# Kernel optimization log

Hardware: AMD Instinct MI355X
Metric: run time of the kernel (lower is better)

The kernel has to match this reference:

```python
import jax, jax.numpy as jnp
import numpy as np

# ---- model dims (match init_kwargs) ----
N_PER = 10000          # nodes per omic view
NUM_OMICS = 3
N = N_PER * NUM_OMICS  # 30000 total nodes (omic blocks are contiguous)
E = 500000             # edges
R = 6                  # num_relations
HEADS = 1
PROJ = 128             # proj_dim
H0 = 128               # hidden_channels[0]
H1 = 128               # hidden_channels[1]
LABELS = 5
IN_SIZES = [2000, 1500, 1000]
SLOPE = 0.2            # RGATConv leaky_relu negative_slope


def setup_inputs() -> dict:
    key = jax.random.key(0)
    ks = iter(jax.random.split(key, 64))

    def nrm(shape, fan_in):
        return jax.random.normal(next(ks), shape, dtype=jnp.float32) / np.float32(np.sqrt(fan_in))

    inp = {}
    for i, s in enumerate(IN_SIZES):
        inp[f"x{i}"] = jax.random.normal(next(ks), (N_PER, s), dtype=jnp.float32)
    for i, s in enumerate(IN_SIZES):
        inp[f"projW{i}"] = nrm((s, PROJ), s)
        inp[f"projb{i}"] = jnp.zeros((PROJ,), jnp.float32)
    for i in range(NUM_OMICS):
        inp[f"slW{i}"] = nrm((PROJ, H0), PROJ)
        inp[f"slb{i}"] = jnp.zeros((H0,), jnp.float32)
    # RGAT layer 1: weight [R, in, heads*out], q/k [heads*out, heads], bias [heads*out]
    inp["W1"] = nrm((R, PROJ, HEADS * H0), PROJ)
    inp["q1"] = nrm((HEADS * H0, HEADS), H0)
    inp["k1"] = nrm((HEADS * H0, HEADS), H0)
    inp["b1"] = jnp.zeros((HEADS * H0,), jnp.float32)
    # RGAT layer 2: heads=1
    inp["W2"] = nrm((R, HEADS * H0, H1), H0)
    inp["q2"] = nrm((H1, 1), H1)
    inp["k2"] = nrm((H1, 1), H1)
    inp["b2"] = jnp.zeros((H1,), jnp.float32)
    inp["lin1W"] = nrm((H1, H1), H1)
    inp["lin1b"] = jnp.zeros((H1,), jnp.float32)
    inp["lin2W"] = nrm((H1, LABELS), H1)
    inp["lin2b"] = jnp.zeros((LABELS,), jnp.float32)
    inp["edge_src"] = jax.random.randint(next(ks), (E,), 0, N, dtype=jnp.int32)
    inp["edge_dst"] = jax.random.randint(next(ks), (E,), 0, N, dtype=jnp.int32)
    inp["edge_type"] = jax.random.randint(next(ks), (E,), 0, R, dtype=jnp.int32)
    return inp


def _rgat(x, src, dst, etype, W, q, k, b, heads, out_ch):
    """PyG RGATConv: additive-self-attention, across-relation softmax, mod='f-scaled'."""
    # per-relation linear transform of all nodes, then gather per edge
    xw = jnp.einsum('nd,rdo->rno', x, W)          # [R, N, heads*out]
    out_i = xw[etype, dst]                        # [E, heads*out] (target)
    out_j = xw[etype, src]                        # [E, heads*out] (source)
    alpha = jax.nn.leaky_relu(out_i @ q + out_j @ k, SLOPE)   # [E, heads]
    # segment softmax over destination nodes
    m = jax.ops.segment_max(alpha, dst, num_segments=N)
    a = jnp.exp(alpha - m[dst])
    s = jax.ops.segment_sum(a, dst, num_segments=N)
    a = a / s[dst]
    # f-scaled: multiply by in-degree of destination
    deg = jax.ops.segment_sum(jnp.ones((a.shape[0],), a.dtype), dst, num_segments=N)
    a = a * deg[dst][:, None]
    msg = (a[:, :, None] * out_j.reshape(-1, heads, out_ch)).reshape(-1, heads * out_ch)
    return jax.ops.segment_sum(msg, dst, num_segments=N) + b


def reference(x0, x1, x2, projW0, projb0, projW1, projb1, projW2, projb2,
              slW0, slb0, slW1, slb1, slW2, slb2,
              W1, q1, k1, b1, W2, q2, k2, b2,
              lin1W, lin1b, lin2W, lin2b,
              edge_src, edge_dst, edge_type):
    # per-omic projections (ELU)
    xp0 = jax.nn.elu(x0 @ projW0 + projb0)
    xp1 = jax.nn.elu(x1 @ projW1 + projb1)
    xp2 = jax.nn.elu(x2 @ projW2 + projb2)
    x = jnp.concatenate([xp0, xp1, xp2], axis=0)  # [N, PROJ] homogeneous features
    # self-loop contributions (self_loops1 is applied after BOTH convs, on projected x,
    # as in the original forward). Omic node blocks are contiguous.
    sl = jnp.concatenate([xp0 @ slW0 + slb0, xp1 @ slW1 + slb1, xp2 @ slW2 + slb2], axis=0)
    h = jax.nn.elu(_rgat(x, edge_src, edge_dst, edge_type, W1, q1, k1, b1, HEADS, H0) + sl)
    h = jax.nn.elu(_rgat(h, edge_src, edge_dst, edge_type, W2, q2, k2, b2, 1, H1) + sl)
    # classify node_type == 0 nodes (first omic block); dropout p=0.2 is identity at eval
    z = jax.nn.elu(h[:N_PER] @ lin1W + lin1b)
    return z @ lin2W + lin2b
```

## Files before the change

kernel.cpp:

```cpp
#include <hip/hip_runtime.h>
#include <math.h>

#define N_TOTAL 30000
#define NPER 10000
#define NEDGE 500000
#define NREL 6
#define SLOPE 0.2f
#define MAXDEG 256

typedef __attribute__((ext_vector_type(4))) float f32x4;
typedef __attribute__((ext_vector_type(8))) short s16x8;
typedef __attribute__((ext_vector_type(4))) short s16x4;
typedef unsigned short u16;
typedef unsigned int u32;

__device__ __forceinline__ u16 f2bf(float v) {
  u32 x = __float_as_uint(v);
  u32 r = (x + 0x7fffu + ((x >> 16) & 1u)) >> 16;
  return (u16)r;
}
__device__ __forceinline__ float bf2f(u16 u) {
  return __uint_as_float(((u32)u) << 16);
}

struct GB {
  const float* A[3];
  const u16* Bt[3];
  const float* bias[3];
  const float* add[3];
  float* C[3];
  int K[3];
  int Kp[3];
};

template<bool BIAS, bool ELU, bool ADD>
__global__ __launch_bounds__(256, 2)
void gemm_mfma(GB gb, int M)
{
  __shared__ char As[64 * 128];
  __shared__ char Aslo[64 * 128];
  __shared__ char Bs[128 * 128];
  const int z = blockIdx.z;
  const int K = gb.K[z], Kp = gb.Kp[z];
  const int tid = threadIdx.x;
  const int bm = blockIdx.x * 64;
  const int lane = tid & 63;
  const int wave = tid >> 6;
  const int wr = wave >> 1, wc = wave & 1;
  const int lane16 = lane & 15, lhalf = lane >> 4;
  const float* A = gb.A[z];
  const u16* Bt = gb.Bt[z];

  f32x4 acc[2][4];
  #pragma unroll
  for (int mi = 0; mi < 2; mi++)
    #pragma unroll
    for (int ni = 0; ni < 4; ni++)
      #pragma unroll
      for (int q = 0; q < 4; q++) acc[mi][ni][q] = 0.f;

  for (int k0 = 0; k0 < Kp; k0 += 64) {
    #pragma unroll
    for (int it = 0; it < 4; it++) {
      int idx = tid + it * 256;
      int row = idx >> 4;
      int kc = (idx & 15) << 2;
      int gr = bm + row, gk = k0 + kc;
      float4 v = make_float4(0.f, 0.f, 0.f, 0.f);
      if (gr < M && gk < K) v = *(const float4*)&A[(size_t)gr * K + gk];
      s16x4 hi, lo;
      float vv[4] = {v.x, v.y, v.z, v.w};
      #pragma unroll
      for (int j = 0; j < 4; j++) {
        u16 h = f2bf(vv[j]);
        hi[j] = (short)h;
        lo[j] = (short)f2bf(vv[j] - bf2f(h));
      }
      int boff = row * 128 + ((kc * 2) ^ ((row & 7) << 4));
      *(s16x4*)(As + boff) = hi;
      *(s16x4*)(Aslo + boff) = lo;
    }
    #pragma unroll
    for (int it = 0; it < 4; it++) {
      int idx = tid + it * 256;
      int row = idx >> 3;
      int kc = (idx & 7) << 3;
      s16x8 v = *(const s16x8*)&Bt[(size_t)row * Kp + k0 + kc];
      *(s16x8*)(Bs + row * 128 + ((kc * 2) ^ ((row & 7) << 4))) = v;
    }
    __syncthreads();
    #pragma unroll
    for (int kk = 0; kk < 2; kk++) {
      const int kbyte = kk * 64 + lhalf * 16;
      s16x8 afh[2], afl[2], bfr[4];
      #pragma unroll
      for (int mi = 0; mi < 2; mi++) {
        int row = wr * 32 + mi * 16 + lane16;
        int boff = row * 128 + (kbyte ^ ((row & 7) << 4));
        afh[mi] = *(const s16x8*)(As + boff);
        afl[mi] = *(const s16x8*)(Aslo + boff);
      }
      #pragma unroll
      for (int ni = 0; ni < 4; ni++) {
        int row = wc * 64 + ni * 16 + lane16;
        bfr[ni] = *(const s16x8*)(Bs + row * 128 + (kbyte ^ ((row & 7) << 4)));
      }
      #pragma unroll
      for (int mi = 0; mi < 2; mi++)
        #pragma unroll
        for (int ni = 0; ni < 4; ni++) {
          acc[mi][ni] = __builtin_amdgcn_mfma_f32_16x16x32_bf16(
              afl[mi], bfr[ni], acc[mi][ni], 0, 0, 0);
          acc[mi][ni] = __builtin_amdgcn_mfma_f32_16x16x32_bf16(
              afh[mi], bfr[ni], acc[mi][ni], 0, 0, 0);
        }
    }
    __syncthreads();
  }

  float bcol[4];
  #pragma unroll
  for (int ni = 0; ni < 4; ni++) {
    int col = wc * 64 + ni * 16 + lane16;
    if (BIAS) bcol[ni] = gb.bias[z][col];
  }
  #pragma unroll
  for (int mi = 0; mi < 2; mi++) {
    #pragma unroll
    for (int q = 0; q < 4; q++) {
      int grow = bm + wr * 32 + mi * 16 + lhalf * 4 + q;
      if (grow < M) {
        #pragma unroll
        for (int ni = 0; ni < 4; ni++) {
          float v = acc[mi][ni][q];
          int col = wc * 64 + ni * 16 + lane16;
          if (BIAS) v += bcol[ni];
          if (ADD) v += gb.add[z][(size_t)grow * 128 + col];
          if (ELU) v = v > 0.f ? v : expm1f(v);
          gb.C[z][(size_t)grow * 128 + col] = v;
        }
      }
    }
  }
}

struct SK {
  const float* A[3];
  const u16* Bt[3];
  float* C[3];
  int K[3];
  int Kp[3];
};

__global__ __launch_bounds__(256, 2)
void gemm_splitk(SK sk, int M)
{
  __shared__ char As[64 * 128];
  __shared__ char Aslo[64 * 128];
  __shared__ char Bs[128 * 128];
  const int z = blockIdx.z;
  const int K = sk.K[z], Kp = sk.Kp[z];
  const int cb = blockIdx.y * 512;
  if (cb >= Kp) return;
  const int kend = (cb + 512 < Kp) ? cb + 512 : Kp;
  const int tid = threadIdx.x;
  const int bm = blockIdx.x * 64;
  const int lane = tid & 63;
  const int wave = tid >> 6;
  const int wr = wave >> 1, wc = wave & 1;
  const int lane16 = lane & 15, lhalf = lane >> 4;
  const float* A = sk.A[z];
  const u16* Bt = sk.Bt[z];

  f32x4 acc[2][4];
  #pragma unroll
  for (int mi = 0; mi < 2; mi++)
    #pragma unroll
    for (int ni = 0; ni < 4; ni++)
      #pragma unroll
      for (int q = 0; q < 4; q++) acc[mi][ni][q] = 0.f;

  for (int k0 = cb; k0 < kend; k0 += 64) {
    #pragma unroll
    for (int it = 0; it < 4; it++) {
      int idx = tid + it * 256;
      int row = idx >> 4;
      int kc = (idx & 15) << 2;
      int gr = bm + row, gk = k0 + kc;
      float4 v = make_float4(0.f, 0.f, 0.f, 0.f);
      if (gr < M && gk < K) v = *(const float4*)&A[(size_t)gr * K + gk];
      s16x4 hi, lo;
      float vv[4] = {v.x, v.y, v.z, v.w};
      #pragma unroll
      for (int j = 0; j < 4; j++) {
        u16 h = f2bf(vv[j]);
        hi[j] = (short)h;
        lo[j] = (short)f2bf(vv[j] - bf2f(h));
      }
      int boff = row * 128 + ((kc * 2) ^ ((row & 7) << 4));
      *(s16x4*)(As + boff) = hi;
      *(s16x4*)(Aslo + boff) = lo;
    }
    #pragma unroll
    for (int it = 0; it < 4; it++) {
      int idx = tid + it * 256;
      int row = idx >> 3;
      int kc = (idx & 7) << 3;
      s16x8 v = *(const s16x8*)&Bt[(size_t)row * Kp + k0 + kc];
      *(s16x8*)(Bs + row * 128 + ((kc * 2) ^ ((row & 7) << 4))) = v;
    }
    __syncthreads();
    #pragma unroll
    for (int kk = 0; kk < 2; kk++) {
      const int kbyte = kk * 64 + lhalf * 16;
      s16x8 afh[2], afl[2], bfr[4];
      #pragma unroll
      for (int mi = 0; mi < 2; mi++) {
        int row = wr * 32 + mi * 16 + lane16;
        int boff = row * 128 + (kbyte ^ ((row & 7) << 4));
        afh[mi] = *(const s16x8*)(As + boff);
        afl[mi] = *(const s16x8*)(Aslo + boff);
      }
      #pragma unroll
      for (int ni = 0; ni < 4; ni++) {
        int row = wc * 64 + ni * 16 + lane16;
        bfr[ni] = *(const s16x8*)(Bs + row * 128 + (kbyte ^ ((row & 7) << 4)));
      }
      #pragma unroll
      for (int mi = 0; mi < 2; mi++)
        #pragma unroll
        for (int ni = 0; ni < 4; ni++) {
          acc[mi][ni] = __builtin_amdgcn_mfma_f32_16x16x32_bf16(
              afl[mi], bfr[ni], acc[mi][ni], 0, 0, 0);
          acc[mi][ni] = __builtin_amdgcn_mfma_f32_16x16x32_bf16(
              afh[mi], bfr[ni], acc[mi][ni], 0, 0, 0);
        }
    }
    __syncthreads();
  }

  float* C = sk.C[z] + (size_t)blockIdx.y * M * 128;
  #pragma unroll
  for (int mi = 0; mi < 2; mi++) {
    #pragma unroll
    for (int q = 0; q < 4; q++) {
      int grow = bm + wr * 32 + mi * 16 + lhalf * 4 + q;
      if (grow < M) {
        #pragma unroll
        for (int ni = 0; ni < 4; ni++) {
          int col = wc * 64 + ni * 16 + lane16;
          C[(size_t)grow * 128 + col] = acc[mi][ni][q];
        }
      }
    }
  }
}

struct RP { const float* bias[3]; int nch[3]; };

__global__ __launch_bounds__(256)
void reduce_proj(const float* __restrict__ part, RP rp, float* __restrict__ Xf)
{
  int z = blockIdx.z;
  int i = blockIdx.x * 256 + threadIdx.x;
  int c = i & 127;
  int nch = rp.nch[z];
  const float* base = part + (size_t)z * 4 * NPER * 128 + i;
  float s = 0.f;
  for (int ch = 0; ch < nch; ch++) s += base[(size_t)ch * NPER * 128];
  s += rp.bias[z][c];
  Xf[(size_t)z * NPER * 128 + i] = s > 0.f ? s : expm1f(s);
}

struct CW {
  const float* src[9];
  u16* dst[9];
  int K[9];
  int Kp[9];
};

__global__ __launch_bounds__(256)
void conv_w(CW cw) {
  int z = blockIdx.z;
  int K = cw.K[z], Kp = cw.Kp[z];
  int idx = blockIdx.x * 256 + threadIdx.x;
  if (idx >= 128 * Kp) return;
  int kq = idx >> 7, n = idx & 127;
  cw.dst[z][(size_t)n * Kp + kq] =
      (kq < K) ? f2bf(cw.src[z][(size_t)kq * 128 + n]) : (u16)0;
}

__global__ __launch_bounds__(128)
void wqk_kernel(const float* __restrict__ W, const float* __restrict__ q,
                const float* __restrict__ k, float* __restrict__ wq,
                float* __restrict__ wk)
{
  int r = blockIdx.x;
  int t = threadIdx.x;
  const float* Wr = W + (size_t)r * 128 * 128 + (size_t)t * 128;
  float aq = 0.f, ak = 0.f;
  for (int o = 0; o < 128; o++) {
    float w = Wr[o];
    aq = fmaf(w, q[o], aq);
    ak = fmaf(w, k[o], ak);
  }
  wq[r * 128 + t] = aq;
  wk[r * 128 + t] = ak;
}

__global__ __launch_bounds__(256)
void qdkd_kernel(const float* __restrict__ Xf, const float* __restrict__ wq,
                 const float* __restrict__ wk, float* __restrict__ QD,
                 float* __restrict__ KD)
{
  __shared__ float sq[NREL * 128], sk[NREL * 128];
  for (int i = threadIdx.x; i < NREL * 128; i += 256) { sq[i] = wq[i]; sk[i] = wk[i]; }
  __syncthreads();
  int n = blockIdx.x * 256 + threadIdx.x;
  if (n >= N_TOTAL) return;
  float aq[NREL], ak[NREL];
  #pragma unroll
  for (int r = 0; r < NREL; r++) { aq[r] = 0.f; ak[r] = 0.f; }
  for (int kc = 0; kc < 128; kc += 4) {
    float4 x = *(const float4*)&Xf[(size_t)n * 128 + kc];
    #pragma unroll
    for (int r = 0; r < NREL; r++) {
      aq[r] += x.x * sq[r * 128 + kc] + x.y * sq[r * 128 + kc + 1]
             + x.z * sq[r * 128 + kc + 2] + x.w * sq[r * 128 + kc + 3];
      ak[r] += x.x * sk[r * 128 + kc] + x.y * sk[r * 128 + kc + 1]
             + x.z * sk[r * 128 + kc + 2] + x.w * sk[r * 128 + kc + 3];
    }
  }
  #pragma unroll
  for (int r = 0; r < NREL; r++) {
    QD[(size_t)r * N_TOTAL + n] = aq[r];
    KD[(size_t)r * N_TOTAL + n] = ak[r];
  }
}

__global__ __launch_bounds__(256)
void edge_count(const int* __restrict__ dst, int* __restrict__ cnt) {
  int e = blockIdx.x * 256 + threadIdx.x;
  if (e < NEDGE) atomicAdd(&cnt[dst[e]], 1);
}

__global__ __launch_bounds__(1024)
void scan_kernel(const int* __restrict__ cnt, int* __restrict__ off,
                 int* __restrict__ cur) {
  __shared__ int ps[1024];
  const int t = threadIdx.x;
  const int CH = (N_TOTAL + 1023) / 1024;
  const int base = t * CH;
  int s = 0;
  for (int i = 0; i < CH; i++) {
    int idx = base + i;
    if (idx < N_TOTAL) s += cnt[idx];
  }
  ps[t] = s;
  __syncthreads();
  for (int o = 1; o < 1024; o <<= 1) {
    int v = (t >= o) ? ps[t - o] : 0;
    __syncthreads();
    ps[t] += v;
    __syncthreads();
  }
  int run = ps[t] - s;
  for (int i = 0; i < CH; i++) {
    int idx = base + i;
    if (idx < N_TOTAL) {
      off[idx] = run; cur[idx] = run;
      run += cnt[idx];
    }
  }
  if (t == 1023) off[N_TOTAL] = run;
}

__global__ __launch_bounds__(256)
void edge_fill(const int* __restrict__ dst, int* __restrict__ cur,
               int* __restrict__ csre) {
  int e = blockIdx.x * 256 + threadIdx.x;
  if (e >= NEDGE) return;
  int p = atomicAdd(&cur[dst[e]], 1);
  csre[p] = e;
}

__device__ __forceinline__ float block_max2(float v, float* red, int tid) {
  #pragma unroll
  for (int m = 32; m; m >>= 1) v = fmaxf(v, __shfl_xor(v, m));
  if ((tid & 63) == 0) red[tid >> 6] = v;
  __syncthreads();
  return fmaxf(red[0], red[1]);
}
__device__ __forceinline__ float block_sum2(float v, float* red, int tid) {
  #pragma unroll
  for (int m = 32; m; m >>= 1) v += __shfl_xor(v, m);
  if ((tid & 63) == 0) red[tid >> 6] = v;
  __syncthreads();
  return red[0] + red[1];
}

__global__ __launch_bounds__(128)
void csr_agg2(const int* __restrict__ off, const int* __restrict__ csre,
              const int* __restrict__ src, const int* __restrict__ et,
              const float* __restrict__ qd, const float* __restrict__ kd,
              const float* __restrict__ xrow, float* __restrict__ agg)
{
  __shared__ float al[MAXDEG];
  __shared__ int2 st[MAXDEG];
  __shared__ float redm[2], reds[2];
  __shared__ float qrow[NREL];
  const int d = blockIdx.x;
  const int tid = threadIdx.x;
  const int n0 = off[d];
  const int deg = off[d + 1] - n0;
  float accr[NREL] = {0.f, 0.f, 0.f, 0.f, 0.f, 0.f};

  if (deg > 0) {
    if (tid < NREL) qrow[tid] = qd[tid * N_TOTAL + d];
    __syncthreads();
    const bool fits = (deg <= MAXDEG);
    float lmax = -3.0e38f;
    for (int i = tid; i < deg; i += 128) {
      int e = csre[n0 + i];
      int t = et[e], s_ = src[e];
      float a = qrow[t] + kd[t * N_TOTAL + s_];
      a = (a > 0.f) ? a : SLOPE * a;
      if (fits) { al[i] = a; st[i] = make_int2(t, s_); }
      lmax = fmaxf(lmax, a);
    }
    __syncthreads();
    const float m = block_max2(lmax, redm, tid);
    float lsum = 0.f;
    for (int i = tid; i < deg; i += 128) {
      float a;
      if (fits) a = al[i];
      else {
        int e = csre[n0 + i];
        a = qrow[et[e]] + kd[et[e] * N_TOTAL + src[e]];
        a = (a > 0.f) ? a : SLOPE * a;
      }
      lsum += expf(a - m);
    }
    const float ssum = block_sum2(lsum, reds, tid);
    const float scale = (float)deg / ssum;
    if (fits) {
      for (int i = tid; i < deg; i += 128)
        al[i] = expf(al[i] - m) * scale;
    }
    __syncthreads();
    if (fits) {
      int i = 0;
      for (; i + 1 < deg; i += 2) {
        float c0 = al[i], c1 = al[i + 1];
        int2 e0 = st[i], e1 = st[i + 1];
        float v0 = xrow[(size_t)e0.y * 128 + tid];
        float v1 = xrow[(size_t)e1.y * 128 + tid];
        float cv0 = c0 * v0, cv1 = c1 * v1;
        #pragma unroll
        for (int r = 0; r < NREL; r++) {
          accr[r] += (e0.x == r) ? cv0 : 0.f;
          accr[r] += (e1.x == r) ? cv1 : 0.f;
        }
      }
      if (i < deg) {
        int2 e0 = st[i];
        float cv0 = al[i] * xrow[(size_t)e0.y * 128 + tid];
        #pragma unroll
        for (int r = 0; r < NREL; r++) accr[r] += (e0.x == r) ? cv0 : 0.f;
      }
    } else {
      for (int i = 0; i < deg; i++) {
        int e = csre[n0 + i];
        int t = et[e], s_ = src[e];
        float a = qrow[t] + kd[t * N_TOTAL + s_];
        a = (a > 0.f) ? a : SLOPE * a;
        float cv = expf(a - m) * scale * xrow[(size_t)s_ * 128 + tid];
        #pragma unroll
        for (int r = 0; r < NREL; r++) accr[r] += (t == r) ? cv : 0.f;
      }
    }
  }
  #pragma unroll
  for (int r = 0; r < NREL; r++)
    agg[((size_t)d * NREL + r) * 128 + tid] = accr[r];
}

__global__ __launch_bounds__(256)
void lin2_kernel(const float* __restrict__ z, const float* __restrict__ W,
                 const float* __restrict__ b, float* __restrict__ out)
{
  int row = blockIdx.x * 4 + (threadIdx.x >> 6);
  int lane = threadIdx.x & 63;
  if (row >= NPER) return;
  float p[5] = {0.f, 0.f, 0.f, 0.f, 0.f};
  #pragma unroll
  for (int h = 0; h < 2; h++) {
    int kidx = lane + h * 64;
    float zv = z[(size_t)row * 128 + kidx];
    #pragma unroll
    for (int j = 0; j < 5; j++) p[j] = fmaf(zv, W[kidx * 5 + j], p[j]);
  }
  #pragma unroll
  for (int mm = 32; mm; mm >>= 1)
    #pragma unroll
    for (int j = 0; j < 5; j++) p[j] += __shfl_xor(p[j], mm);
  if (lane == 0) {
    #pragma unroll
    for (int j = 0; j < 5; j++) out[(size_t)row * 5 + j] = p[j] + b[j];
  }
}

extern "C" void kernel_launch(void* const* d_in, const int* in_sizes, int n_in,
                              void* d_out, int out_size, void* d_ws, size_t ws_size,
                              hipStream_t stream) {
  const float* xs[3] = {(const float*)d_in[0], (const float*)d_in[1], (const float*)d_in[2]};
  const float* projW[3] = {(const float*)d_in[3], (const float*)d_in[5], (const float*)d_in[7]};
  const float* projb[3] = {(const float*)d_in[4], (const float*)d_in[6], (const float*)d_in[8]};
  const float* slW[3]   = {(const float*)d_in[9], (const float*)d_in[11], (const float*)d_in[13]};
  const float* slb[3]   = {(const float*)d_in[10], (const float*)d_in[12], (const float*)d_in[14]};
  const float* W1 = (const float*)d_in[15];
  const float* q1 = (const float*)d_in[16];
  const float* k1 = (const float*)d_in[17];
  const float* b1 = (const float*)d_in[18];
  const float* W2 = (const float*)d_in[19];
  const float* q2 = (const float*)d_in[20];
  const float* k2 = (const float*)d_in[21];
  const float* b2 = (const float*)d_in[22];
  const float* lin1W = (const float*)d_in[23];
  const float* lin1b = (const float*)d_in[24];
  const float* lin2W = (const float*)d_in[25];
  const float* lin2b = (const float*)d_in[26];
  const int* esrc = (const int*)d_in[27];
  const int* edst = (const int*)d_in[28];
  const int* etyp = (const int*)d_in[29];

  char* wp = (char*)d_ws;
  auto alloc = [&](size_t bytes) -> char* {
    char* p = wp; wp += (bytes + 255) & ~(size_t)255; return p;
  };
  float* Xf  = (float*)alloc((size_t)N_TOTAL * 128 * 4);
  float* SL  = (float*)alloc((size_t)N_TOTAL * 128 * 4);
  float* Hf  = (float*)alloc((size_t)N_TOTAL * 128 * 4);
  float* QD  = (float*)alloc((size_t)NREL * N_TOTAL * 4);
  float* KD  = (float*)alloc((size_t)NREL * N_TOTAL * 4);
  float* Z   = (float*)alloc((size_t)NPER * 128 * 4);
  float* WQ1 = (float*)alloc((size_t)NREL * 128 * 4);
  float* WK1 = (float*)alloc((size_t)NREL * 128 * 4);
  float* WQ2 = (float*)alloc((size_t)NREL * 128 * 4);
  float* WK2 = (float*)alloc((size_t)NREL * 128 * 4);
  int*   CNT = (int*)  alloc((size_t)N_TOTAL * 4);
  int*   OFF = (int*)  alloc((size_t)(N_TOTAL + 1) * 4);
  int*   CUR = (int*)  alloc((size_t)N_TOTAL * 4);
  int*   CSRE= (int*)  alloc((size_t)NEDGE * 4);

  float* AGG  = (float*)alloc((size_t)N_TOTAL * NREL * 128 * 4);
  float* PART = AGG;

  CW cw;
  int nW = 0;
  auto addW = [&](const float* src, int K) {
    int Kp = (K + 63) & ~63;
    cw.src[nW] = src; cw.K[nW] = K; cw.Kp[nW] = Kp;
    cw.dst[nW] = (u16*)alloc((size_t)128 * Kp * 2);
    nW++;
  };
  addW(projW[0], 2000); addW(projW[1], 1500); addW(projW[2], 1000);
  addW(slW[0], 128); addW(slW[1], 128); addW(slW[2], 128);
  addW(W1, NREL * 128);
  addW(W2, NREL * 128);
  addW(lin1W, 128);

  const int gridM_per = (NPER + 63) / 64;
  const int gridM_tot = (N_TOTAL + 63) / 64;
  const int gridE = (NEDGE + 255) / 256;

  hipMemsetAsync(CNT, 0, (size_t)N_TOTAL * 4, stream);
  edge_count<<<gridE, 256, 0, stream>>>(edst, CNT);
  scan_kernel<<<1, 1024, 0, stream>>>(CNT, OFF, CUR);
  edge_fill<<<gridE, 256, 0, stream>>>(edst, CUR, CSRE);

  conv_w<<<dim3(1024, 1, 9), 256, 0, stream>>>(cw);
  wqk_kernel<<<NREL, 128, 0, stream>>>(W1, q1, k1, WQ1, WK1);
  wqk_kernel<<<NREL, 128, 0, stream>>>(W2, q2, k2, WQ2, WK2);

  {
    SK sk;
    for (int z = 0; z < 3; z++) {
      sk.A[z] = xs[z]; sk.Bt[z] = cw.dst[z];
      sk.C[z] = PART + (size_t)z * 4 * NPER * 128;
      sk.K[z] = cw.K[z]; sk.Kp[z] = cw.Kp[z];
    }
    gemm_splitk<<<dim3(gridM_per, 4, 3), 256, 0, stream>>>(sk, NPER);
    RP rp;
    for (int z = 0; z < 3; z++) { rp.bias[z] = projb[z]; rp.nch[z] = cw.Kp[z] / 512; }
    reduce_proj<<<dim3(NPER * 128 / 256, 1, 3), 256, 0, stream>>>(PART, rp, Xf);
  }
  {
    GB g;
    for (int z = 0; z < 3; z++) {
      g.A[z] = Xf + (size_t)z * NPER * 128; g.Bt[z] = cw.dst[3 + z];
      g.bias[z] = slb[z]; g.add[z] = nullptr;
      g.C[z] = SL + (size_t)z * NPER * 128;
      g.K[z] = 128; g.Kp[z] = 128;
    }
    gemm_mfma<true, false, false><<<dim3(gridM_per, 1, 3), 256, 0, stream>>>(g, NPER);
  }

  for (int layer = 0; layer < 2; layer++) {
    const float* Ain = (layer == 0) ? Xf : Hf;
    const float* WQ = (layer == 0) ? WQ1 : WQ2;
    const float* WK = (layer == 0) ? WK1 : WK2;
    const float* bb = (layer == 0) ? b1 : b2;
    const u16* Wstk = cw.dst[6 + layer];

    qdkd_kernel<<<(N_TOTAL + 255) / 256, 256, 0, stream>>>(Ain, WQ, WK, QD, KD);
    csr_agg2<<<N_TOTAL, 128, 0, stream>>>(OFF, CSRE, esrc, etyp, QD, KD, Ain, AGG);
    GB g;
    g.A[0] = AGG; g.Bt[0] = Wstk; g.bias[0] = bb; g.add[0] = SL; g.C[0] = Hf;
    g.K[0] = NREL * 128; g.Kp[0] = NREL * 128;
    gemm_mfma<true, true, true><<<dim3(gridM_tot, 1, 1), 256, 0, stream>>>(g, N_TOTAL);
  }

  {
    GB g;
    g.A[0] = Hf; g.Bt[0] = cw.dst[8]; g.bias[0] = lin1b; g.add[0] = nullptr; g.C[0] = Z;
    g.K[0] = 128; g.Kp[0] = 128;
    gemm_mfma<true, true, false><<<dim3(gridM_per, 1, 1), 256, 0, stream>>>(g, NPER);
  }
  lin2_kernel<<<(NPER + 3) / 4, 256, 0, stream>>>(Z, lin2W, lin2b, (float*)d_out);
}
```

Before: 501.9 us.

## Prefetch GEMM tiles into registers, pack edge metadata, wave-per-node aggregation

The GEMM body moves into a shared core that loads the next K-tile from global memory into registers while the current tile is computed, overlapping memory latency with MFMA work. The CSR fill now stores the source index and edge type packed into one int, which removes the indirect loads of src and etype during aggregation. Aggregation switches from one 128-thread block per node to one 64-lane wave per node, with wave-level shuffles for the softmax and float2 feature loads, so no shared memory or block barriers are needed. The packing assumes node ids fit in 15 bits; 30000 does, but only just. Adds register pressure, and degrees above 256 take a slower three-pass path.

Result: faster. 432.9 us (-13.7%).

```diff
diff --git a/kernel.cpp b/kernel.cpp
--- a/kernel.cpp
+++ b/kernel.cpp
@@ -6,7 +6,7 @@
 #define NEDGE 500000
 #define NREL 6
 #define SLOPE 0.2f
-#define MAXDEG 256
+#define WCAP 4
 
 typedef __attribute__((ext_vector_type(4))) float f32x4;
 typedef __attribute__((ext_vector_type(8))) short s16x8;
@@ -21,6 +21,133 @@
 }
 __device__ __forceinline__ float bf2f(u16 u) {
   return __uint_as_float(((u32)u) << 16);
+}
+
+template<bool BIAS, bool ELU, bool ADD, bool SPLITK>
+__device__ __forceinline__ void gemm_core(
+    const float* __restrict__ A, const u16* __restrict__ Bt,
+    const float* __restrict__ bias, const float* __restrict__ add,
+    float* __restrict__ C, int M, int K, int Kp, int kbeg, int kend)
+{
+  __shared__ char As[64 * 128];
+  __shared__ char Aslo[64 * 128];
+  __shared__ char Bs[128 * 128];
+  const int tid = threadIdx.x;
+  const int bm = blockIdx.x * 64;
+  const int lane = tid & 63;
+  const int wave = tid >> 6;
+  const int wr = wave >> 1, wc = wave & 1;
+  const int lane16 = lane & 15, lhalf = lane >> 4;
+
+  const int a_row0 = tid >> 4;
+  const int a_kc = (tid & 15) << 2;
+  const int b_row0 = tid >> 3;
+  const int b_kc = (tid & 7) << 3;
+
+  float4 pa[4];
+  s16x8 pb[4];
+
+  auto LOAD = [&](int k0) {
+    #pragma unroll
+    for (int it = 0; it < 4; it++) {
+      int gr = bm + a_row0 + it * 16, gk = k0 + a_kc;
+      float4 v = make_float4(0.f, 0.f, 0.f, 0.f);
+      if (gr < M && gk < K) v = *(const float4*)&A[(size_t)gr * K + gk];
+      pa[it] = v;
+    }
+    #pragma unroll
+    for (int it = 0; it < 4; it++) {
+      int row = b_row0 + it * 32;
+      pb[it] = *(const s16x8*)&Bt[(size_t)row * Kp + k0 + b_kc];
+    }
+  };
+
+  f32x4 acc[2][4];
+  #pragma unroll
+  for (int mi = 0; mi < 2; mi++)
+    #pragma unroll
+    for (int ni = 0; ni < 4; ni++)
+      #pragma unroll
+      for (int q = 0; q < 4; q++) acc[mi][ni][q] = 0.f;
+
+  LOAD(kbeg);
+
+  for (int k0 = kbeg; k0 < kend; k0 += 64) {
+    #pragma unroll
+    for (int it = 0; it < 4; it++) {
+      int row = a_row0 + it * 16;
+      float vv[4] = {pa[it].x, pa[it].y, pa[it].z, pa[it].w};
+      s16x4 hi, lo;
+      #pragma unroll
+      for (int j = 0; j < 4; j++) {
+        u16 h = f2bf(vv[j]);
+        hi[j] = (short)h;
+        lo[j] = (short)f2bf(vv[j] - bf2f(h));
+      }
+      int boff = row * 128 + ((a_kc * 2) ^ ((row & 7) << 4));
+      *(s16x4*)(As + boff) = hi;
+      *(s16x4*)(Aslo + boff) = lo;
+    }
+    #pragma unroll
+    for (int it = 0; it < 4; it++) {
+      int row = b_row0 + it * 32;
+      *(s16x8*)(Bs + row * 128 + ((b_kc * 2) ^ ((row & 7) << 4))) = pb[it];
+    }
+    __syncthreads();
+    if (k0 + 64 < kend) LOAD(k0 + 64);
+    #pragma unroll
+    for (int kk = 0; kk < 2; kk++) {
+      const int kbyte = kk * 64 + lhalf * 16;
+      s16x8 afh[2], afl[2], bfr[4];
+      #pragma unroll
+      for (int mi = 0; mi < 2; mi++) {
+        int row = wr * 32 + mi * 16 + lane16;
+        int boff = row * 128 + (kbyte ^ ((row & 7) << 4));
+        afh[mi] = *(const s16x8*)(As + boff);
+        afl[mi] = *(const s16x8*)(Aslo + boff);
+      }
+      #pragma unroll
+      for (int ni = 0; ni < 4; ni++) {
+        int row = wc * 64 + ni * 16 + lane16;
+        bfr[ni] = *(const s16x8*)(Bs + row * 128 + (kbyte ^ ((row & 7) << 4)));
+      }
+      #pragma unroll
+      for (int mi = 0; mi < 2; mi++)
+        #pragma unroll
+        for (int ni = 0; ni < 4; ni++) {
+          acc[mi][ni] = __builtin_amdgcn_mfma_f32_16x16x32_bf16(
+              afl[mi], bfr[ni], acc[mi][ni], 0, 0, 0);
+          acc[mi][ni] = __builtin_amdgcn_mfma_f32_16x16x32_bf16(
+              afh[mi], bfr[ni], acc[mi][ni], 0, 0, 0);
+        }
+    }
+    __syncthreads();
+  }
+
+  float bcol[4];
+  #pragma unroll
+  for (int ni = 0; ni < 4; ni++) {
+    int col = wc * 64 + ni * 16 + lane16;
+    if (BIAS) bcol[ni] = bias[col];
+  }
+  #pragma unroll
+  for (int mi = 0; mi < 2; mi++) {
+    #pragma unroll
+    for (int q = 0; q < 4; q++) {
+      int grow = bm + wr * 32 + mi * 16 + lhalf * 4 + q;
+      if (grow < M) {
+        #pragma unroll
+        for (int ni = 0; ni < 4; ni++) {
+          float v = acc[mi][ni][q];
+          int col = wc * 64 + ni * 16 + lane16;
+          if (BIAS) v += bcol[ni];
+          if (ADD) v += add[(size_t)grow * 128 + col];
+          if (!SPLITK && ELU) v = v > 0.f ? v : expm1f(v);
+          C[(size_t)grow * 128 + col] = v;
+        }
+      }
+    }
+  }
 }
 
 struct GB {
@@ -37,111 +164,9 @@
 __global__ __launch_bounds__(256, 2)
 void gemm_mfma(GB gb, int M)
 {
-  __shared__ char As[64 * 128];
-  __shared__ char Aslo[64 * 128];
-  __shared__ char Bs[128 * 128];
-  const int z = blockIdx.z;
-  const int K = gb.K[z], Kp = gb.Kp[z];
-  const int tid = threadIdx.x;
-  const int bm = blockIdx.x * 64;
-  const int lane = tid & 63;
-  const int wave = tid >> 6;
-  const int wr = wave >> 1, wc = wave & 1;
-  const int lane16 = lane & 15, lhalf = lane >> 4;
-  const float* A = gb.A[z];
-  const u16* Bt = gb.Bt[z];
-
-  f32x4 acc[2][4];
-  #pragma unroll
-  for (int mi = 0; mi < 2; mi++)
-    #pragma unroll
-    for (int ni = 0; ni < 4; ni++)
-      #pragma unroll
-      for (int q = 0; q < 4; q++) acc[mi][ni][q] = 0.f;
-
-  for (int k0 = 0; k0 < Kp; k0 += 64) {
-    #pragma unroll
-    for (int it = 0; it < 4; it++) {
-      int idx = tid + it * 256;
-      int row = idx >> 4;
-      int kc = (idx & 15) << 2;
-      int gr = bm + row, gk = k0 + kc;
-      float4 v = make_float4(0.f, 0.f, 0.f, 0.f);
-      if (gr < M && gk < K) v = *(const float4*)&A[(size_t)gr * K + gk];
-      s16x4 hi, lo;
-      float vv[4] = {v.x, v.y, v.z, v.w};
-      #pragma unroll
-      for (int j = 0; j < 4; j++) {
-        u16 h = f2bf(vv[j]);
-        hi[j] = (short)h;
-        lo[j] = (short)f2bf(vv[j] - bf2f(h));
-      }
-      int boff = row * 128 + ((kc * 2) ^ ((row & 7) << 4));
-      *(s16x4*)(As + boff) = hi;
-      *(s16x4*)(Aslo + boff) = lo;
-    }
-    #pragma unroll
-    for (int it = 0; it < 4; it++) {
-      int idx = tid + it * 256;
-      int row = idx >> 3;
-      int kc = (idx & 7) << 3;
-      s16x8 v = *(const s16x8*)&Bt[(size_t)row * Kp + k0 + kc];
-      *(s16x8*)(Bs + row * 128 + ((kc * 2) ^ ((row & 7) << 4))) = v;
-    }
-    __syncthreads();
-    #pragma unroll
-    for (int kk = 0; kk < 2; kk++) {
-      const int kbyte = kk * 64 + lhalf * 16;
-      s16x8 afh[2], afl[2], bfr[4];
-      #pragma unroll
-      for (int mi = 0; mi < 2; mi++) {
-        int row = wr * 32 + mi * 16 + lane16;
-        int boff = row * 128 + (kbyte ^ ((row & 7) << 4));
-        afh[mi] = *(const s16x8*)(As + boff);
-        afl[mi] = *(const s16x8*)(Aslo + boff);
-      }
-      #pragma unroll
-      for (int ni = 0; ni < 4; ni++) {
-        int row = wc * 64 + ni * 16 + lane16;
-        bfr[ni] = *(const s16x8*)(Bs + row * 128 + (kbyte ^ ((row & 7) << 4)));
-      }
-      #pragma unroll
-      for (int mi = 0; mi < 2; mi++)
-        #pragma unroll
-        for (int ni = 0; ni < 4; ni++) {
-          acc[mi][ni] = __builtin_amdgcn_mfma_f32_16x16x32_bf16(
-              afl[mi], bfr[ni], acc[mi][ni], 0, 0, 0);
-          acc[mi][ni] = __builtin_amdgcn_mfma_f32_16x16x32_bf16(
-              afh[mi], bfr[ni], acc[mi][ni], 0, 0, 0);
-        }
-    }
-    __syncthreads();
-  }
-
-  float bcol[4];
-  #pragma unroll
-  for (int ni = 0; ni < 4; ni++) {
-    int col = wc * 64 + ni * 16 + lane16;
-    if (BIAS) bcol[ni] = gb.bias[z][col];
-  }
-  #pragma unroll
-  for (int mi = 0; mi < 2; mi++) {
-    #pragma unroll
-    for (int q = 0; q < 4; q++) {
-      int grow = bm + wr * 32 + mi * 16 + lhalf * 4 + q;
-      if (grow < M) {
-        #pragma unroll
-        for (int ni = 0; ni < 4; ni++) {
-          float v = acc[mi][ni][q];
-          int col = wc * 64 + ni * 16 + lane16;
-          if (BIAS) v += bcol[ni];
-          if (ADD) v += gb.add[z][(size_t)grow * 128 + col];
-          if (ELU) v = v > 0.f ? v : expm1f(v);
-          gb.C[z][(size_t)grow * 128 + col] = v;
-        }
-      }
-    }
-  }
+  int z = blockIdx.z;
+  gemm_core<BIAS, ELU, ADD, false>(gb.A[z], gb.Bt[z], gb.bias[z], gb.add[z],
+                                   gb.C[z], M, gb.K[z], gb.Kp[z], 0, gb.Kp[z]);
 }
 
 struct SK {
@@ -155,105 +180,13 @@
 __global__ __launch_bounds__(256, 2)
 void gemm_splitk(SK sk, int M)
 {
-  __shared__ char As[64 * 128];
-  __shared__ char Aslo[64 * 128];
-  __shared__ char Bs[128 * 128];
-  const int z = blockIdx.z;
-  const int K = sk.K[z], Kp = sk.Kp[z];
-  const int cb = blockIdx.y * 512;
-  if (cb >= Kp) return;
-  const int kend = (cb + 512 < Kp) ? cb + 512 : Kp;
-  const int tid = threadIdx.x;
-  const int bm = blockIdx.x * 64;
-  const int lane = tid & 63;
-  const int wave = tid >> 6;
-  const int wr = wave >> 1, wc = wave & 1;
-  const int lane16 = lane & 15, lhalf = lane >> 4;
-  const float* A = sk.A[z];
-  const u16* Bt = sk.Bt[z];
-
-  f32x4 acc[2][4];
-  #pragma unroll
-  for (int mi = 0; mi < 2; mi++)
-    #pragma unroll
-    for (int ni = 0; ni < 4; ni++)
-      #pragma unroll
-      for (int q = 0; q < 4; q++) acc[mi][ni][q] = 0.f;
-
-  for (int k0 = cb; k0 < kend; k0 += 64) {
-    #pragma unroll
-    for (int it = 0; it < 4; it++) {
-      int idx = tid + it * 256;
-      int row = idx >> 4;
-      int kc = (idx & 15) << 2;
-      int gr = bm + row, gk = k0 + kc;
-      float4 v = make_float4(0.f, 0.f, 0.f, 0.f);
-      if (gr < M && gk < K) v = *(const float4*)&A[(size_t)gr * K + gk];
-      s16x4 hi, lo;
-      float vv[4] = {v.x, v.y, v.z, v.w};
-      #pragma unroll
-      for (int j = 0; j < 4; j++) {
-        u16 h = f2bf(vv[j]);
-        hi[j] = (short)h;
-        lo[j] = (short)f2bf(vv[j] - bf2f(h));
-      }
-      int boff = row * 128 + ((kc * 2) ^ ((row & 7) << 4));
-      *(s16x4*)(As + boff) = hi;
-      *(s16x4*)(Aslo + boff) = lo;
-    }
-    #pragma unroll
-    for (int it = 0; it < 4; it++) {
-      int idx = tid + it * 256;
-      int row = idx >> 3;
-      int kc = (idx & 7) << 3;
-      s16x8 v = *(const s16x8*)&Bt[(size_t)row * Kp + k0 + kc];
-      *(s16x8*)(Bs + row * 128 + ((kc * 2) ^ ((row & 7) << 4))) = v;
-    }
-    __syncthreads();
-    #pragma unroll
-    for (int kk = 0; kk < 2; kk++) {
-      const int kbyte = kk * 64 + lhalf * 16;
-      s16x8 afh[2], afl[2], bfr[4];
-      #pragma unroll
-      for (int mi = 0; mi < 2; mi++) {
-        int row = wr * 32 + mi * 16 + lane16;
-        int boff = row * 128 + (kbyte ^ ((row & 7) << 4));
-        afh[mi] = *(const s16x8*)(As + boff);
-        afl[mi] = *(const s16x8*)(Aslo + boff);
-      }
-      #pragma unroll
-      for (int ni = 0; ni < 4; ni++) {
-        int row = wc * 64 + ni * 16 + lane16;
-        bfr[ni] = *(const s16x8*)(Bs + row * 128 + (kbyte ^ ((row & 7) << 4)));
-      }
-      #pragma unroll
-      for (int mi = 0; mi < 2; mi++)
-        #pragma unroll
-        for (int ni = 0; ni < 4; ni++) {
-          acc[mi][ni] = __builtin_amdgcn_mfma_f32_16x16x32_bf16(
-              afl[mi], bfr[ni], acc[mi][ni], 0, 0, 0);
-          acc[mi][ni] = __builtin_amdgcn_mfma_f32_16x16x32_bf16(
-              afh[mi], bfr[ni], acc[mi][ni], 0, 0, 0);
-        }
-    }
-    __syncthreads();
-  }
-
+  int z = blockIdx.z;
+  int cb = blockIdx.y * 512;
+  if (cb >= sk.Kp[z]) return;
+  int kend = (cb + 512 < sk.Kp[z]) ? cb + 512 : sk.Kp[z];
   float* C = sk.C[z] + (size_t)blockIdx.y * M * 128;
-  #pragma unroll
-  for (int mi = 0; mi < 2; mi++) {
-    #pragma unroll
-    for (int q = 0; q < 4; q++) {
-      int grow = bm + wr * 32 + mi * 16 + lhalf * 4 + q;
-      if (grow < M) {
-        #pragma unroll
-        for (int ni = 0; ni < 4; ni++) {
-          int col = wc * 64 + ni * 16 + lane16;
-          C[(size_t)grow * 128 + col] = acc[mi][ni][q];
-        }
-      }
-    }
-  }
+  gemm_core<false, false, false, true>(sk.A[z], sk.Bt[z], nullptr, nullptr,
+                                       C, M, sk.K[z], sk.Kp[z], cb, kend);
 }
 
 struct RP { const float* bias[3]; int nch[3]; };
@@ -376,113 +309,123 @@
 }
 
 __global__ __launch_bounds__(256)
-void edge_fill(const int* __restrict__ dst, int* __restrict__ cur,
-               int* __restrict__ csre) {
+void edge_fill(const int* __restrict__ dst, const int* __restrict__ src,
+               const int* __restrict__ et, int* __restrict__ cur,
+               int* __restrict__ meta) {
   int e = blockIdx.x * 256 + threadIdx.x;
   if (e >= NEDGE) return;
   int p = atomicAdd(&cur[dst[e]], 1);
-  csre[p] = e;
-}
-
-__device__ __forceinline__ float block_max2(float v, float* red, int tid) {
-  #pragma unroll
-  for (int m = 32; m; m >>= 1) v = fmaxf(v, __shfl_xor(v, m));
-  if ((tid & 63) == 0) red[tid >> 6] = v;
-  __syncthreads();
-  return fmaxf(red[0], red[1]);
-}
-__device__ __forceinline__ float block_sum2(float v, float* red, int tid) {
-  #pragma unroll
-  for (int m = 32; m; m >>= 1) v += __shfl_xor(v, m);
-  if ((tid & 63) == 0) red[tid >> 6] = v;
-  __syncthreads();
-  return red[0] + red[1];
-}
-
-__global__ __launch_bounds__(128)
-void csr_agg2(const int* __restrict__ off, const int* __restrict__ csre,
-              const int* __restrict__ src, const int* __restrict__ et,
+  meta[p] = src[e] | (et[e] << 15);
+}
+
+__global__ __launch_bounds__(256)
+void csr_aggw(const int* __restrict__ off, const int* __restrict__ meta,
               const float* __restrict__ qd, const float* __restrict__ kd,
               const float* __restrict__ xrow, float* __restrict__ agg)
 {
-  __shared__ float al[MAXDEG];
-  __shared__ int2 st[MAXDEG];
-  __shared__ float redm[2], reds[2];
-  __shared__ float qrow[NREL];
-  const int d = blockIdx.x;
-  const int tid = threadIdx.x;
+  const int d = blockIdx.x * 4 + (threadIdx.x >> 6);
+  const int lane = threadIdx.x & 63;
+  if (d >= N_TOTAL) return;
   const int n0 = off[d];
   const int deg = off[d + 1] - n0;
-  float accr[NREL] = {0.f, 0.f, 0.f, 0.f, 0.f, 0.f};
+
+  float2 accr[NREL];
+  #pragma unroll
+  for (int r = 0; r < NREL; r++) accr[r] = make_float2(0.f, 0.f);
+
+  float qrow[NREL];
+  #pragma unroll
+  for (int r = 0; r < NREL; r++) qrow[r] = qd[r * N_TOTAL + d];
 
   if (deg > 0) {
-    if (tid < NREL) qrow[tid] = qd[tid * N_TOTAL + d];
-    __syncthreads();
-    const bool fits = (deg <= MAXDEG);
-    float lmax = -3.0e38f;
-    for (int i = tid; i < deg; i += 128) {
-      int e = csre[n0 + i];
-      int t = et[e], s_ = src[e];
-      float a = qrow[t] + kd[t * N_TOTAL + s_];
-      a = (a > 0.f) ? a : SLOPE * a;
-      if (fits) { al[i] = a; st[i] = make_int2(t, s_); }
-      lmax = fmaxf(lmax, a);
-    }
-    __syncthreads();
-    const float m = block_max2(lmax, redm, tid);
-    float lsum = 0.f;
-    for (int i = tid; i < deg; i += 128) {
-      float a;
-      if (fits) a = al[i];
-      else {
-        int e = csre[n0 + i];
-        a = qrow[et[e]] + kd[et[e] * N_TOTAL + src[e]];
-        a = (a > 0.f) ? a : SLOPE * a;
-      }
-      lsum += expf(a - m);
-    }
-    const float ssum = block_sum2(lsum, reds, tid);
-    const float scale = (float)deg / ssum;
-    if (fits) {
-      for (int i = tid; i < deg; i += 128)
-        al[i] = expf(al[i] - m) * scale;
-    }
-    __syncthreads();
-    if (fits) {
-      int i = 0;
-      for (; i + 1 < deg; i += 2) {
-        float c0 = al[i], c1 = al[i + 1];
-        int2 e0 = st[i], e1 = st[i + 1];
-        float v0 = xrow[(size_t)e0.y * 128 + tid];
-        float v1 = xrow[(size_t)e1.y * 128 + tid];
-        float cv0 = c0 * v0, cv1 = c1 * v1;
+    if (deg <= 64 * WCAP) {
+      int mreg[WCAP];
+      float areg[WCAP];
+      const int nc = (deg + 63) >> 6;
+      float lmax = -3.0e38f;
+      #pragma unroll
+      for (int c = 0; c < WCAP; c++) {
+        mreg[c] = 0; areg[c] = -3.0e38f;
+        int i = c * 64 + lane;
+        if (c < nc && i < deg) {
+          int mm = meta[n0 + i];
+          int s_ = mm & 0x7FFF, t = mm >> 15;
+          float a = qrow[t] + kd[t * N_TOTAL + s_];
+          a = (a > 0.f) ? a : SLOPE * a;
+          mreg[c] = mm; areg[c] = a;
+          lmax = fmaxf(lmax, a);
+        }
+      }
+      #pragma unroll
+      for (int m = 32; m; m >>= 1) lmax = fmaxf(lmax, __shfl_xor(lmax, m));
+      float lsum = 0.f;
+      #pragma unroll
+      for (int c = 0; c < WCAP; c++) {
+        int i = c * 64 + lane;
+        if (c < nc && i < deg) {
+          areg[c] = expf(areg[c] - lmax);
+          lsum += areg[c];
+        }
+      }
+      #pragma unroll
+      for (int m = 32; m; m >>= 1) lsum += __shfl_xor(lsum, m);
+      const float scale = (float)deg / lsum;
+      for (int i = 0; i < deg; i++) {
+        int c = i >> 6, l = i & 63;
+        float cf = 0.f; int mm = 0;
+        #pragma unroll
+        for (int cc = 0; cc < WCAP; cc++) {
+          if (cc == c) { cf = __shfl(areg[cc], l); mm = __shfl(mreg[cc], l); }
+        }
+        cf *= scale;
+        int s_ = mm & 0x7FFF, t = mm >> 15;
+        float2 v = *(const float2*)&xrow[(size_t)s_ * 128 + lane * 2];
+        float2 cv = make_float2(cf * v.x, cf * v.y);
         #pragma unroll
         for (int r = 0; r < NREL; r++) {
-          accr[r] += (e0.x == r) ? cv0 : 0.f;
-          accr[r] += (e1.x == r) ? cv1 : 0.f;
-        }
-      }
-      if (i < deg) {
-        int2 e0 = st[i];
-        float cv0 = al[i] * xrow[(size_t)e0.y * 128 + tid];
-        #pragma unroll
-        for (int r = 0; r < NREL; r++) accr[r] += (e0.x == r) ? cv0 : 0.f;
+          bool hit = (t == r);
+          accr[r].x += hit ? cv.x : 0.f;
+          accr[r].y += hit ? cv.y : 0.f;
+        }
       }
     } else {
+      float m = -3.0e38f;
       for (int i = 0; i < deg; i++) {
-        int e = csre[n0 + i];
-        int t = et[e], s_ = src[e];
+        int mm = meta[n0 + i];
+        int s_ = mm & 0x7FFF, t = mm >> 15;
         float a = qrow[t] + kd[t * N_TOTAL + s_];
         a = (a > 0.f) ? a : SLOPE * a;
-        float cv = expf(a - m) * scale * xrow[(size_t)s_ * 128 + tid];
+        m = fmaxf(m, a);
+      }
+      float ssum = 0.f;
+      for (int i = 0; i < deg; i++) {
+        int mm = meta[n0 + i];
+        int s_ = mm & 0x7FFF, t = mm >> 15;
+        float a = qrow[t] + kd[t * N_TOTAL + s_];
+        a = (a > 0.f) ? a : SLOPE * a;
+        ssum += expf(a - m);
+      }
+      const float scale = (float)deg / ssum;
+      for (int i = 0; i < deg; i++) {
+        int mm = meta[n0 + i];
+        int s_ = mm & 0x7FFF, t = mm >> 15;
+        float a = qrow[t] + kd[t * N_TOTAL + s_];
+        a = (a > 0.f) ? a : SLOPE * a;
+        float cf = expf(a - m) * scale;
+        float2 v = *(const float2*)&xrow[(size_t)s_ * 128 + lane * 2];
+        float2 cv = make_float2(cf * v.x, cf * v.y);
         #pragma unroll
-        for (int r = 0; r < NREL; r++) accr[r] += (t == r) ? cv : 0.f;
+        for (int r = 0; r < NREL; r++) {
+          bool hit = (t == r);
+          accr[r].x += hit ? cv.x : 0.f;
+          accr[r].y += hit ? cv.y : 0.f;
+        }
       }
     }
   }
   #pragma unroll
   for (int r = 0; r < NREL; r++)
-    agg[((size_t)d * NREL + r) * 128 + tid] = accr[r];
+    *(float2*)&agg[((size_t)d * NREL + r) * 128 + lane * 2] = accr[r];
 }
 
 __global__ __launch_bounds__(256)
@@ -551,7 +494,7 @@
   int*   CNT = (int*)  alloc((size_t)N_TOTAL * 4);
   int*   OFF = (int*)  alloc((size_t)(N_TOTAL + 1) * 4);
   int*   CUR = (int*)  alloc((size_t)N_TOTAL * 4);
-  int*   CSRE= (int*)  alloc((size_t)NEDGE * 4);
+  int*   META= (int*)  alloc((size_t)NEDGE * 4);
 
   float* AGG  = (float*)alloc((size_t)N_TOTAL * NREL * 128 * 4);
   float* PART = AGG;
@@ -577,7 +520,7 @@
   hipMemsetAsync(CNT, 0, (size_t)N_TOTAL * 4, stream);
   edge_count<<<gridE, 256, 0, stream>>>(edst, CNT);
   scan_kernel<<<1, 1024, 0, stream>>>(CNT, OFF, CUR);
-  edge_fill<<<gridE, 256, 0, stream>>>(edst, CUR, CSRE);
+  edge_fill<<<gridE, 256, 0, stream>>>(edst, esrc, etyp, CUR, META);
 
   conv_w<<<dim3(1024, 1, 9), 256, 0, stream>>>(cw);
   wqk_kernel<<<NREL, 128, 0, stream>>>(W1, q1, k1, WQ1, WK1);
@@ -614,7 +557,7 @@
     const u16* Wstk = cw.dst[6 + layer];
 
     qdkd_kernel<<<(N_TOTAL + 255) / 256, 256, 0, stream>>>(Ain, WQ, WK, QD, KD);
-    csr_agg2<<<N_TOTAL, 128, 0, stream>>>(OFF, CSRE, esrc, etyp, QD, KD, Ain, AGG);
+    csr_aggw<<<(N_TOTAL + 3) / 4, 256, 0, stream>>>(OFF, META, QD, KD, Ain, AGG);
     GB g;
     g.A[0] = AGG; g.Bt[0] = Wstk; g.bias[0] = bb; g.add[0] = SL; g.C[0] = Hf;
     g.K[0] = NREL * 128; g.Kp[0] = NREL * 128;
```
